# Optimization experiments

Hardware: AMD Instinct MI355X
Metric: run time of the kernel (lower is better)

## Reference

```python
import jax, jax.numpy as jnp
import numpy as np


def setup_inputs() -> dict:
    key = jax.random.key(0)
    N, L, S, H, E = 2, 2048, 2048, 8, 64
    k0, k1, k2, k3 = jax.random.split(key, 4)
    queries = jax.random.normal(k0, (N, L, H, E), dtype=jnp.float32)
    keys = jax.random.normal(k1, (N, S, H, E), dtype=jnp.float32)
    values = jax.random.normal(k2, (N, S, H, E), dtype=jnp.float32)
    Erel = jax.random.normal(k3, (L, E), dtype=jnp.float32)  # self.E relative embedding table
    # causal additive mask: 0 where key <= query, -1e9 elsewhere
    attn_mask_add = jnp.where(jnp.arange(S)[None, :] <= jnp.arange(L)[:, None], 0.0, -1e9).astype(jnp.float32)
    key_len_add = jnp.zeros((N, S), dtype=jnp.float32)  # full-length sequences
    return {"queries": queries, "keys": keys, "values": values, "Erel": Erel,
            "attn_mask_add": attn_mask_add, "key_len_add": key_len_add}


def reference(queries, keys, values, Erel, attn_mask_add, key_len_add):
    N, L, H, E = queries.shape
    S = keys.shape[1]
    temp = 1.0 / np.sqrt(E)
    q = (queries * temp).transpose(0, 2, 1, 3)   # [N,H,L,E]
    k = keys.transpose(0, 2, 1, 3)               # [N,H,S,E]
    # relative logits: QE [N,H,L,M], M = L (E table has L rows)
    QE = jnp.einsum('nhle,me->nhlm', q, Erel)
    M = QE.shape[-1]
    # _qe_masking: keep qe[i, j] where j >= M - 1 - i
    i = jnp.arange(L)[:, None]
    j = jnp.arange(M)[None, :]
    QE = QE * (j >= (M - 1 - i)).astype(QE.dtype)
    # _skewing: pad one zero column on the left, reshape swapping last two dims, drop first row
    padded = jnp.pad(QE, ((0, 0), (0, 0), (0, 0), (1, 0)))          # [N,H,L,M+1]
    Srel = padded.reshape(N, H, M + 1, L)[:, :, 1:, :]               # [N,H,M,L] == [N,H,L,S] since M==L==S
    QK = (jnp.einsum('nhle,nhse->nhls', q, k)
          + Srel
          + attn_mask_add[None, None, :, :]
          + key_len_add[:, None, None, :])
    A = jax.nn.softmax(QK, axis=-1)  # dropout disabled (eval-mode reference)
    V = jnp.einsum('nhls,nshd->nlhd', A, values)
    return V
```

## Files before the change

kernel.cpp:

```cpp
#include <hip/hip_runtime.h>
#include <hip/hip_bf16.h>


typedef __attribute__((ext_vector_type(8))) short bf16x8;
typedef __attribute__((ext_vector_type(4))) float f32x4;
typedef unsigned short u16;

#define L_Q 2048
#define S_K 2048
#define N_H 8
#define E_D 64
#define RSTRIDE 512
#define LOG2E 1.44269504088896f

#define QW_OFF 0u
#define KW_OFF (4u << 20)
#define VT_OFF (8u << 20)
#define EW_OFF (12u << 20)
#define ML_OFF (13u << 20)
#define OW_OFF ((13u << 20) + (512u << 10))
#define WS_PACK ((size_t)(13u << 20))
#define WS_FULL ((size_t)OW_OFF + (size_t)1024 * 4096 * 4)

static __device__ __forceinline__ short f2bf(float f) {
  unsigned u = __builtin_bit_cast(unsigned, f);
  u += 0x7fffu + ((u >> 16) & 1u);
  return (short)(u >> 16);
}

static __device__ __forceinline__ unsigned pk2(float a, float b) {
  return (unsigned)(u16)f2bf(a) | ((unsigned)(u16)f2bf(b) << 16);
}

static __device__ __forceinline__ bf16x8 loadpack8(const float* __restrict__ p, float scale) {
  float4 a = *reinterpret_cast<const float4*>(p);
  float4 b = *reinterpret_cast<const float4*>(p + 4);
  bf16x8 r;
  r[0] = f2bf(a.x * scale); r[1] = f2bf(a.y * scale);
  r[2] = f2bf(a.z * scale); r[3] = f2bf(a.w * scale);
  r[4] = f2bf(b.x * scale); r[5] = f2bf(b.y * scale);
  r[6] = f2bf(b.z * scale); r[7] = f2bf(b.w * scale);
  return r;
}

__global__ __launch_bounds__(256)
void pack_qke(const float* __restrict__ Qf, const float* __restrict__ Kf,
              const float* __restrict__ Ef, u16* __restrict__ Qw,
              u16* __restrict__ Kw, u16* __restrict__ Ew) {
  const unsigned u = blockIdx.x * 256 + threadIdx.x;
  if (u < 1048576u) {
    const unsigned v  = u & 524287u;
    const int e  = (v & 15) * 4;
    const int i  = (v >> 4) & 2047;
    const int nh = v >> 15;
    const int n = nh >> 3, h = nh & 7;
    const size_t src = ((size_t)(n * L_Q + i) * N_H + h) * E_D + e;
    const size_t dst = ((size_t)nh * L_Q + i) * E_D + e;
    const bool isQ = u < 524288u;
    float4 x = *reinterpret_cast<const float4*>((isQ ? Qf : Kf) + src);
    const float s = isQ ? 0.125f * LOG2E : 1.0f;
    ushort4 o;
    o.x = (u16)f2bf(x.x * s); o.y = (u16)f2bf(x.y * s);
    o.z = (u16)f2bf(x.z * s); o.w = (u16)f2bf(x.w * s);
    *reinterpret_cast<ushort4*>((isQ ? Qw : Kw) + dst) = o;
  } else {
    const unsigned v = u - 1048576u;
    if (v < 32768u) {
      const size_t idx = (size_t)v * 4;
      float4 x = *reinterpret_cast<const float4*>(Ef + idx);
      ushort4 o;
      o.x = (u16)f2bf(x.x); o.y = (u16)f2bf(x.y);
      o.z = (u16)f2bf(x.z); o.w = (u16)f2bf(x.w);
      *reinterpret_cast<ushort4*>(Ew + idx) = o;
    }
  }
}

__global__ __launch_bounds__(256)
void pack_vt(const float* __restrict__ Vf, u16* __restrict__ Vtw) {
  __shared__ u16 t[64][72];
  const int j0 = blockIdx.x * 64;
  const int nh = blockIdx.y;
  const int n = nh >> 3, h = nh & 7;
  const int tid = threadIdx.x;
  {
    const int jr = tid >> 2, dg = (tid & 3) * 16;
    const float* src = Vf + ((size_t)(n * L_Q + j0 + jr) * N_H + h) * E_D + dg;
#pragma unroll
    for (int q = 0; q < 4; ++q) {
      float4 x = *reinterpret_cast<const float4*>(src + q * 4);
      t[jr][dg + q * 4 + 0] = (u16)f2bf(x.x);
      t[jr][dg + q * 4 + 1] = (u16)f2bf(x.y);
      t[jr][dg + q * 4 + 2] = (u16)f2bf(x.z);
      t[jr][dg + q * 4 + 3] = (u16)f2bf(x.w);
    }
  }
  __syncthreads();
  {
    const int dr = tid >> 2, jg = (tid & 3) * 16;
    u16 tmp[16];
#pragma unroll
    for (int jj = 0; jj < 16; ++jj) tmp[jj] = t[jg + jj][dr];
    u16* dst = Vtw + ((size_t)nh * E_D + dr) * S_K + j0 + jg;
    *reinterpret_cast<uint4*>(dst)     = *reinterpret_cast<uint4*>(&tmp[0]);
    *reinterpret_cast<uint4*>(dst + 8) = *reinterpret_cast<uint4*>(&tmp[8]);
  }
}

template <bool SPLIT>
__global__ __launch_bounds__(256, 3)
void relattn_r11(const u16* __restrict__ Qw, const u16* __restrict__ Kw,
                 const u16* __restrict__ Vtw, const u16* __restrict__ Ew,
                 const float* __restrict__ KLp, float* __restrict__ Op,
                 float* __restrict__ OwP, float* __restrict__ MLp) {
  const int bid = blockIdx.x;
  const int nh = bid & 15;
  const int n = nh >> 3, h = nh & 7;
  const int rest = bid >> 4;
  const int wq64 = SPLIT ? (31 - (rest >> 1))
                         : ((rest < 16) ? (31 - rest) : (rest - 16));
  const int sp = SPLIT ? (rest & 1) : 0;
  const int iw64 = wq64 * 64;
  const int tid = threadIdx.x;
  const int wid = tid >> 6;
  const int lane = tid & 63;
  const int lo = lane & 15, hi = lane >> 4;
  const int iw = iw64 + wid * 16;
  const int nt = wq64 + 1;
  const int t0 = (SPLIT && sp) ? (nt >> 1) : 0;
  const int t1 = (SPLIT && !sp) ? (nt >> 1) : nt;
  const int s = (wq64 * 16 + nh) * 2 + sp;

  __shared__ u16 Kls[2][64 * 64];
  __shared__ u16 Vls[2][64 * 64];
  __shared__ float qe_lds[4][16 * 80];

  if (SPLIT && t0 >= t1) {
    f32x4 z = {};
    f32x4* OwF = reinterpret_cast<f32x4*>(OwP) + (size_t)s * 1024 + wid * 256 + lane;
#pragma unroll
    for (int dt = 0; dt < 4; ++dt) OwF[dt * 64] = z;
    if (lane < 16) {
      MLp[s * 128 + wid * 32 + lane] = -1e30f;
      MLp[s * 128 + wid * 32 + 16 + lane] = 0.f;
    }
    return;
  }

  const u16* Kg = Kw + (size_t)nh * S_K * E_D;
  const u16* Vg = Vtw + (size_t)nh * E_D * S_K;
  const float* klq = KLp + (size_t)n * S_K + 4 * hi;
  const u16* epl = Ew + (size_t)(2032 - iw) * E_D + lo * E_D + hi * 8;

  const int srow = lane >> 3;
  const int scc  = lane & 7;
  const int r0 = wid * 8 + srow;
  const int r1 = r0 + 32;
  const int swc = (scc ^ srow) * 8;
  uint4 stK[2], stV[2];

  auto LOAD_KV = [&](int jj0) {
    stK[0] = *reinterpret_cast<const uint4*>(Kg + (size_t)(jj0 + r0) * E_D + scc * 8);
    stK[1] = *reinterpret_cast<const uint4*>(Kg + (size_t)(jj0 + r1) * E_D + scc * 8);
    stV[0] = *reinterpret_cast<const uint4*>(Vg + (size_t)r0 * S_K + jj0 + scc * 8);
    stV[1] = *reinterpret_cast<const uint4*>(Vg + (size_t)r1 * S_K + jj0 + scc * 8);
  };
  auto WRITE_KV = [&](int bb) {
    *reinterpret_cast<uint4*>(&Kls[bb][r0 * 64 + swc]) = stK[0];
    *reinterpret_cast<uint4*>(&Kls[bb][r1 * 64 + swc]) = stK[1];
    *reinterpret_cast<uint4*>(&Vls[bb][r0 * 64 + swc]) = stV[0];
    *reinterpret_cast<uint4*>(&Vls[bb][r1 * 64 + swc]) = stV[1];
  };

  bf16x8 efc[8];
  auto LOAD_EFC = [&](int tt64) {
#pragma unroll
    for (int kt = 0; kt < 2; ++kt)
#pragma unroll
      for (int tt = 1; tt < 5; ++tt)
        efc[kt * 4 + tt - 1] = *reinterpret_cast<const bf16x8*>(
            epl + (size_t)(tt64 * 64 + tt * 16) * E_D + kt * 32);
  };

  bf16x8 qa[2];
  {
    const u16* qrow = Qw + ((size_t)nh * L_Q + iw + lo) * E_D + hi * 8;
    qa[0] = *reinterpret_cast<const bf16x8*>(qrow);
    qa[1] = *reinterpret_cast<const bf16x8*>(qrow + 32);
  }

  LOAD_KV(t0 * 64);
  WRITE_KV(0);
  if (t0 + 1 < t1) LOAD_KV((t0 + 1) * 64);
  LOAD_EFC(t0);
  __syncthreads();

  f32x4 o_acc[4] = {};
  float m_run = -1e30f, l_run = 0.f;
  const float* rb = &qe_lds[wid][lo * 80 + (15 - lo) + 4 * hi];
  const int lsw = lo & 7;
  int b = 0;
  f32x4 qe_carry = {};

  for (int t = t0; t < t1; ++t) {
    const int j0 = t * 64;
    if (t + 1 < t1) WRITE_KV(b ^ 1);
    if (t + 2 < t1) LOAD_KV(j0 + 128);

    __builtin_amdgcn_s_setprio(1);
    f32x4 s_acc[4] = {};
#pragma unroll
    for (int kt = 0; kt < 2; ++kt)
#pragma unroll
      for (int ct = 0; ct < 4; ++ct) {
        const bf16x8 kf = *reinterpret_cast<const bf16x8*>(
            &Kls[b][(ct * 16 + lo) * 64 + (((kt * 4 + hi) ^ lsw) * 8)]);
        s_acc[ct] = __builtin_amdgcn_mfma_f32_16x16x32_bf16(kf, qa[kt], s_acc[ct], 0, 0, 0);
      }

    f32x4 qe_acc[5];
    if (t == t0) {
      f32x4 z = {};
      qe_acc[0] = z;
#pragma unroll
      for (int kt = 0; kt < 2; ++kt) {
        const bf16x8 e0 = *reinterpret_cast<const bf16x8*>(
            epl + (size_t)(t0 * 64) * E_D + kt * 32);
        qe_acc[0] = __builtin_amdgcn_mfma_f32_16x16x32_bf16(e0, qa[kt], qe_acc[0], 0, 0, 0);
      }
    } else {
      qe_acc[0] = qe_carry;
    }
#pragma unroll
    for (int tt = 1; tt < 5; ++tt) { f32x4 z = {}; qe_acc[tt] = z; }
#pragma unroll
    for (int kt = 0; kt < 2; ++kt)
#pragma unroll
      for (int tt = 1; tt < 5; ++tt)
        qe_acc[tt] = __builtin_amdgcn_mfma_f32_16x16x32_bf16(efc[kt * 4 + tt - 1], qa[kt],
                                                             qe_acc[tt], 0, 0, 0);
    qe_carry = qe_acc[4];
    __builtin_amdgcn_s_setprio(0);

    if (t + 1 < t1) LOAD_EFC(t + 1);

#pragma unroll
    for (int tt = 0; tt < 5; ++tt)
      *reinterpret_cast<f32x4*>(&qe_lds[wid][lo * 80 + tt * 16 + 4 * hi]) = qe_acc[tt];

    float4 klv[4];
#pragma unroll
    for (int ct = 0; ct < 4; ++ct)
      klv[ct] = *reinterpret_cast<const float4*>(klq + j0 + ct * 16);

    const bool maskt = (t == nt - 1);
    const int thr = iw + lo - j0 - 4 * hi;
    float p[4][4];
#pragma unroll
    for (int ct = 0; ct < 4; ++ct) {
      const float k0 = klv[ct].x * LOG2E, k1 = klv[ct].y * LOG2E;
      const float k2 = klv[ct].z * LOG2E, k3 = klv[ct].w * LOG2E;
      p[ct][0] = s_acc[ct][0] + rb[ct * 16 + 0] + k0;
      p[ct][1] = s_acc[ct][1] + rb[ct * 16 + 1] + k1;
      p[ct][2] = s_acc[ct][2] + rb[ct * 16 + 2] + k2;
      p[ct][3] = s_acc[ct][3] + rb[ct * 16 + 3] + k3;
      if (maskt) {
#pragma unroll
        for (int g = 0; g < 4; ++g)
          if (ct * 16 + g > thr) p[ct][g] = -1e30f;
      }
    }

    float a0 = fmaxf(fmaxf(p[0][0], p[0][1]), fmaxf(p[0][2], p[0][3]));
    float a1 = fmaxf(fmaxf(p[1][0], p[1][1]), fmaxf(p[1][2], p[1][3]));
    float a2 = fmaxf(fmaxf(p[2][0], p[2][1]), fmaxf(p[2][2], p[2][3]));
    float a3 = fmaxf(fmaxf(p[3][0], p[3][1]), fmaxf(p[3][2], p[3][3]));
    float tmax = fmaxf(fmaxf(a0, a1), fmaxf(a2, a3));
    tmax = fmaxf(tmax, __shfl_xor(tmax, 16));
    tmax = fmaxf(tmax, __shfl_xor(tmax, 32));
    const float mnew = fmaxf(m_run, tmax);
    const float alpha = exp2f(m_run - mnew);
#pragma unroll
    for (int ct = 0; ct < 4; ++ct)
#pragma unroll
      for (int g = 0; g < 4; ++g)
        p[ct][g] = exp2f(p[ct][g] - mnew);
    float s0 = (p[0][0] + p[0][1]) + (p[0][2] + p[0][3]);
    float s1 = (p[1][0] + p[1][1]) + (p[1][2] + p[1][3]);
    float s2 = (p[2][0] + p[2][1]) + (p[2][2] + p[2][3]);
    float s3 = (p[3][0] + p[3][1]) + (p[3][2] + p[3][3]);
    float rs = (s0 + s1) + (s2 + s3);
    rs += __shfl_xor(rs, 16);
    rs += __shfl_xor(rs, 32);
    l_run = l_run * alpha + rs;
    m_run = mnew;

#pragma unroll
    for (int dt = 0; dt < 4; ++dt) o_acc[dt] = o_acc[dt] * alpha;

    uint4 w0, w1;
    w0.x = pk2(p[0][0], p[0][1]); w0.y = pk2(p[0][2], p[0][3]);
    w0.z = pk2(p[1][0], p[1][1]); w0.w = pk2(p[1][2], p[1][3]);
    w1.x = pk2(p[2][0], p[2][1]); w1.y = pk2(p[2][2], p[2][3]);
    w1.z = pk2(p[3][0], p[3][1]); w1.w = pk2(p[3][2], p[3][3]);
    const bf16x8 pb0 = __builtin_bit_cast(bf16x8, w0);
    const bf16x8 pb1 = __builtin_bit_cast(bf16x8, w1);

    __builtin_amdgcn_s_setprio(1);
#pragma unroll
    for (int kt = 0; kt < 2; ++kt)
#pragma unroll
      for (int dt = 0; dt < 4; ++dt) {
        const int vrow = dt * 16 + lo;
        const int ch = kt * 4 + (hi >> 1);
        const uint2 va2 = *reinterpret_cast<const uint2*>(
            &Vls[b][vrow * 64 + ((ch ^ lsw) * 8) + (hi & 1) * 4]);
        const uint2 vb2 = *reinterpret_cast<const uint2*>(
            &Vls[b][vrow * 64 + (((ch + 2) ^ lsw) * 8) + (hi & 1) * 4]);
        uint4 uw; uw.x = va2.x; uw.y = va2.y; uw.z = vb2.x; uw.w = vb2.y;
        const bf16x8 vf = __builtin_bit_cast(bf16x8, uw);
        o_acc[dt] = __builtin_amdgcn_mfma_f32_16x16x32_bf16(vf, kt ? pb1 : pb0, o_acc[dt], 0, 0, 0);
      }
    __builtin_amdgcn_s_setprio(0);

    __syncthreads();
    b ^= 1;
  }

  if (SPLIT) {
    f32x4* OwF = reinterpret_cast<f32x4*>(OwP) + (size_t)s * 1024 + wid * 256 + lane;
#pragma unroll
    for (int dt = 0; dt < 4; ++dt) OwF[dt * 64] = o_acc[dt];
    if (lane < 16) {
      MLp[s * 128 + wid * 32 + lane] = m_run;
      MLp[s * 128 + wid * 32 + 16 + lane] = l_run;
    }
  } else {
    const float inv = 1.f / l_run;
    float* ob = Op + (size_t)n * L_Q * RSTRIDE + h * E_D + (size_t)(iw + lo) * RSTRIDE;
#pragma unroll
    for (int dt = 0; dt < 4; ++dt) {
      f32x4 o = o_acc[dt] * inv;
      *reinterpret_cast<f32x4*>(ob + dt * 16 + 4 * hi) = o;
    }
  }
}

__global__ __launch_bounds__(256)
void combine64(const float* __restrict__ OwP, const float* __restrict__ MLp,
               float* __restrict__ Op) {
  const int pair = blockIdx.x;
  const int nh = pair & 15;
  const int wq64 = pair >> 4;
  const int n = nh >> 3, h = nh & 7;
  const int tid = threadIdx.x;
  const int wid = tid >> 6;
  const int lane = tid & 63;
  const int lo = lane & 15, hi = lane >> 4;
  const int s0 = pair * 2, s1 = s0 + 1;
  const float m0 = MLp[s0 * 128 + wid * 32 + lo], l0 = MLp[s0 * 128 + wid * 32 + 16 + lo];
  const float m1 = MLp[s1 * 128 + wid * 32 + lo], l1 = MLp[s1 * 128 + wid * 32 + 16 + lo];
  const float M  = fmaxf(m0, m1);
  const float w0 = exp2f(m0 - M), w1 = exp2f(m1 - M);
  const float inv = 1.f / (l0 * w0 + l1 * w1);
  const f32x4* A = reinterpret_cast<const f32x4*>(OwP) + (size_t)s0 * 1024 + wid * 256 + lane;
  const f32x4* B = reinterpret_cast<const f32x4*>(OwP) + (size_t)s1 * 1024 + wid * 256 + lane;
  float* ob = Op + (size_t)n * L_Q * RSTRIDE + h * E_D
            + (size_t)(wq64 * 64 + wid * 16 + lo) * RSTRIDE;
#pragma unroll
  for (int dt = 0; dt < 4; ++dt) {
    f32x4 o = (A[dt * 64] * w0 + B[dt * 64] * w1) * inv;
    *reinterpret_cast<f32x4*>(ob + dt * 16 + 4 * hi) = o;
  }
}

__global__ __launch_bounds__(64, 2)
void relattn_fb(const float* __restrict__ Qf, const float* __restrict__ Kf,
                const float* __restrict__ Vf, const float* __restrict__ Ef,
                const float* __restrict__ KLp, float* __restrict__ Op) {
  const int bid = blockIdx.x;
  const int nh = bid & 15;
  const int n = nh >> 3, h = nh & 7;
  const int wq = 127 - (bid >> 4);
  const int iw = wq * 16;
  const int lane = threadIdx.x & 63;
  const int lo = lane & 15, hi = lane >> 4;

  __shared__ u16 p_lds[16 * 72];

  const float* klp = KLp + (size_t)n * S_K;
  float* ob = Op + (size_t)n * L_Q * RSTRIDE + h * E_D;

  bf16x8 qa[2];
  const float* qb = Qf + ((size_t)(n * L_Q + iw + lo) * N_H + h) * E_D + hi * 8;
  qa[0] = loadpack8(qb, 0.125f);
  qa[1] = loadpack8(qb + 32, 0.125f);

  f32x4 o_acc[4] = {};
  float m_run[4], l_run[4];
#pragma unroll
  for (int g = 0; g < 4; ++g) { m_run[g] = -1e30f; l_run[g] = 0.f; }

  const int ntiles = (wq >> 2) + 1;
  for (int t = 0; t < ntiles; ++t) {
    const int j0 = t * 64;
    f32x4 s_acc[4] = {};
#pragma unroll
    for (int kt = 0; kt < 2; ++kt)
#pragma unroll
      for (int ct = 0; ct < 4; ++ct) {
        bf16x8 kf = loadpack8(Kf + ((size_t)(n * S_K + j0 + ct * 16 + lo) * N_H + h) * E_D
                                  + kt * 32 + hi * 8, 1.f);
        s_acc[ct] = __builtin_amdgcn_mfma_f32_16x16x32_bf16(qa[kt], kf, s_acc[ct], 0, 0, 0);
      }
    const int mbase = (L_Q - 1) - (iw + 15) + j0;
    f32x4 qe_acc[5] = {};
#pragma unroll
    for (int kt = 0; kt < 2; ++kt)
#pragma unroll
      for (int tt = 0; tt < 5; ++tt) {
        int mr = mbase + tt * 16 + lo;
        mr = mr > (L_Q - 1) ? (L_Q - 1) : mr;
        bf16x8 ef = loadpack8(Ef + (size_t)mr * E_D + kt * 32 + hi * 8, 1.f);
        qe_acc[tt] = __builtin_amdgcn_mfma_f32_16x16x32_bf16(qa[kt], ef, qe_acc[tt], 0, 0, 0);
      }
    float kladd[4];
#pragma unroll
    for (int ct = 0; ct < 4; ++ct) kladd[ct] = klp[j0 + ct * 16 + lo];
    float sv[4][4];
#pragma unroll
    for (int ct = 0; ct < 4; ++ct) {
      const int jj = ct * 16 + lo;
#pragma unroll
      for (int g = 0; g < 4; ++g) {
        const int r = 4 * hi + g;
        const int u = jj - r + 15;
        const int srcl = (u & 15) | (hi << 4);
        const float a = __shfl(qe_acc[ct][g], srcl);
        const float bq = __shfl(qe_acc[ct + 1][g], srcl);
        const float rel = (lo <= r) ? a : bq;
        float sv2 = s_acc[ct][g] + rel + kladd[ct];
        if (j0 + jj > iw + r) sv2 = -1e9f;
        sv[ct][g] = sv2;
      }
    }
    float alpha[4];
#pragma unroll
    for (int g = 0; g < 4; ++g) {
      float mx = fmaxf(fmaxf(sv[0][g], sv[1][g]), fmaxf(sv[2][g], sv[3][g]));
      mx = fmaxf(mx, __shfl_xor(mx, 1));
      mx = fmaxf(mx, __shfl_xor(mx, 2));
      mx = fmaxf(mx, __shfl_xor(mx, 4));
      mx = fmaxf(mx, __shfl_xor(mx, 8));
      const float mnew = fmaxf(m_run[g], mx);
      const float al = __expf(m_run[g] - mnew);
      float rsv = 0.f;
#pragma unroll
      for (int ct = 0; ct < 4; ++ct) {
        const float pv = __expf(sv[ct][g] - mnew);
        sv[ct][g] = pv;
        rsv += pv;
      }
      rsv += __shfl_xor(rsv, 1);
      rsv += __shfl_xor(rsv, 2);
      rsv += __shfl_xor(rsv, 4);
      rsv += __shfl_xor(rsv, 8);
      l_run[g] = l_run[g] * al + rsv;
      m_run[g] = mnew;
      alpha[g] = al;
    }
#pragma unroll
    for (int dt = 0; dt < 4; ++dt)
#pragma unroll
      for (int g = 0; g < 4; ++g)
        o_acc[dt][g] *= alpha[g];
#pragma unroll
    for (int ct = 0; ct < 4; ++ct)
#pragma unroll
      for (int g = 0; g < 4; ++g)
        p_lds[(4 * hi + g) * 72 + ct * 16 + lo] = (u16)f2bf(sv[ct][g]);
#pragma unroll
    for (int jt = 0; jt < 2; ++jt) {
      const bf16x8 pav = *reinterpret_cast<const bf16x8*>(&p_lds[lo * 72 + jt * 32 + hi * 8]);
#pragma unroll
      for (int dt = 0; dt < 4; ++dt) {
        bf16x8 vf;
        const float* vp = Vf + ((size_t)(n * S_K + j0 + jt * 32 + hi * 8) * N_H + h) * E_D
                            + dt * 16 + lo;
#pragma unroll
        for (int e = 0; e < 8; ++e) vf[e] = f2bf(vp[(size_t)e * RSTRIDE]);
        o_acc[dt] = __builtin_amdgcn_mfma_f32_16x16x32_bf16(pav, vf, o_acc[dt], 0, 0, 0);
      }
    }
  }
  float inv[4];
#pragma unroll
  for (int g = 0; g < 4; ++g) inv[g] = 1.f / l_run[g];
#pragma unroll
  for (int dt = 0; dt < 4; ++dt)
#pragma unroll
    for (int g = 0; g < 4; ++g)
      ob[(size_t)(iw + 4 * hi + g) * RSTRIDE + dt * 16 + lo] = o_acc[dt][g] * inv[g];
}

extern "C" void kernel_launch(void* const* d_in, const int* in_sizes, int n_in,
                              void* d_out, int out_size, void* d_ws, size_t ws_size,
                              hipStream_t stream) {
  const float* Q  = (const float*)d_in[0];
  const float* K  = (const float*)d_in[1];
  const float* V  = (const float*)d_in[2];
  const float* E  = (const float*)d_in[3];
  const float* KL = (const float*)d_in[5];
  float* O = (float*)d_out;

  char* ws = (char*)d_ws;
  u16* Qw   = (u16*)(ws + QW_OFF);
  u16* Kw   = (u16*)(ws + KW_OFF);
  u16* Vtw  = (u16*)(ws + VT_OFF);
  u16* Ew   = (u16*)(ws + EW_OFF);
  float* ML = (float*)(ws + ML_OFF);
  float* Ow = (float*)(ws + OW_OFF);

  const bool ws_pack = ws_size >= WS_PACK;
  const bool ws_full = ws_size >= WS_FULL;

  if (ws_pack) {
    hipLaunchKernelGGL(pack_qke, dim3((1048576 + 32768 + 255) / 256), dim3(256), 0, stream,
                       Q, K, E, Qw, Kw, Ew);
    hipLaunchKernelGGL(pack_vt, dim3(32, 16), dim3(256), 0, stream, V, Vtw);
  }
  if (ws_full) {
    hipLaunchKernelGGL((relattn_r11<true>), dim3(1024), dim3(256), 0, stream,
                       Qw, Kw, Vtw, Ew, KL, O, Ow, ML);
    hipLaunchKernelGGL(combine64, dim3(512), dim3(256), 0, stream, Ow, ML, O);
  } else if (ws_pack) {
    hipLaunchKernelGGL((relattn_r11<false>), dim3(512), dim3(256), 0, stream,
                       Qw, Kw, Vtw, Ew, KL, O, Ow, ML);
  } else {
    hipLaunchKernelGGL(relattn_fb, dim3(2048), dim3(64), 0, stream, Q, K, V, E, KL, O);
  }
}
```

Baseline: 93.57 us.

## Move the loop barrier mid-iteration and prefetch key-length bias one tile ahead

All V fragment reads from LDS now happen before a new mid-iteration barrier. That barrier waits on lgkmcnt and replaces the trailing __syncthreads, so each loop iteration has one barrier placed where its wait can overlap softmax work. The key-length bias for the next tile is also loaded one iteration early into registers. The cost is 16 extra uint2 registers holding V fragments plus the prefetched bias, which could push register pressure past the 3-blocks-per-CU launch bound.

New measurement: 104.9 us. 1.12x slower.

```diff
diff --git a/kernel.cpp b/kernel.cpp
--- a/kernel.cpp
+++ b/kernel.cpp
@@ -21,6 +21,13 @@
 #define OW_OFF ((13u << 20) + (512u << 10))
 #define WS_PACK ((size_t)(13u << 20))
 #define WS_FULL ((size_t)OW_OFF + (size_t)1024 * 4096 * 4)
+
+static __device__ __forceinline__ void barrier_lgkm() {
+  asm volatile("s_waitcnt lgkmcnt(0)" ::: "memory");
+  __builtin_amdgcn_sched_barrier(0);
+  __builtin_amdgcn_s_barrier();
+  __builtin_amdgcn_sched_barrier(0);
+}
 
 static __device__ __forceinline__ short f2bf(float f) {
   unsigned u = __builtin_bit_cast(unsigned, f);
@@ -109,7 +116,7 @@
 
 template <bool SPLIT>
 __global__ __launch_bounds__(256, 3)
-void relattn_r11(const u16* __restrict__ Qw, const u16* __restrict__ Kw,
+void relattn_r12(const u16* __restrict__ Qw, const u16* __restrict__ Kw,
                  const u16* __restrict__ Vtw, const u16* __restrict__ Ew,
                  const float* __restrict__ KLp, float* __restrict__ Op,
                  float* __restrict__ OwP, float* __restrict__ MLp) {
@@ -182,6 +189,13 @@
             epl + (size_t)(tt64 * 64 + tt * 16) * E_D + kt * 32);
   };
 
+  float4 klvn[4];
+  auto LOAD_KLV = [&](int jj0) {
+#pragma unroll
+    for (int ct = 0; ct < 4; ++ct)
+      klvn[ct] = *reinterpret_cast<const float4*>(klq + jj0 + ct * 16);
+  };
+
   bf16x8 qa[2];
   {
     const u16* qrow = Qw + ((size_t)nh * L_Q + iw + lo) * E_D + hi * 8;
@@ -193,7 +207,8 @@
   WRITE_KV(0);
   if (t0 + 1 < t1) LOAD_KV((t0 + 1) * 64);
   LOAD_EFC(t0);
-  __syncthreads();
+  LOAD_KLV(t0 * 64);
+  barrier_lgkm();
 
   f32x4 o_acc[4] = {};
   float m_run = -1e30f, l_run = 0.f;
@@ -248,10 +263,25 @@
     for (int tt = 0; tt < 5; ++tt)
       *reinterpret_cast<f32x4*>(&qe_lds[wid][lo * 80 + tt * 16 + 4 * hi]) = qe_acc[tt];
 
+    uint2 vva[8], vvb[8];
+#pragma unroll
+    for (int kt = 0; kt < 2; ++kt)
+#pragma unroll
+      for (int dt = 0; dt < 4; ++dt) {
+        const int vrow = dt * 16 + lo;
+        const int ch = kt * 4 + (hi >> 1);
+        vva[kt * 4 + dt] = *reinterpret_cast<const uint2*>(
+            &Vls[b][vrow * 64 + ((ch ^ lsw) * 8) + (hi & 1) * 4]);
+        vvb[kt * 4 + dt] = *reinterpret_cast<const uint2*>(
+            &Vls[b][vrow * 64 + (((ch + 2) ^ lsw) * 8) + (hi & 1) * 4]);
+      }
+
     float4 klv[4];
 #pragma unroll
-    for (int ct = 0; ct < 4; ++ct)
-      klv[ct] = *reinterpret_cast<const float4*>(klq + j0 + ct * 16);
+    for (int ct = 0; ct < 4; ++ct) klv[ct] = klvn[ct];
+    if (t + 1 < t1) LOAD_KLV(j0 + 64);
+
+    barrier_lgkm();
 
     const bool maskt = (t == nt - 1);
     const int thr = iw + lo - j0 - 4 * hi;
@@ -311,19 +341,14 @@
     for (int kt = 0; kt < 2; ++kt)
 #pragma unroll
       for (int dt = 0; dt < 4; ++dt) {
-        const int vrow = dt * 16 + lo;
-        const int ch = kt * 4 + (hi >> 1);
-        const uint2 va2 = *reinterpret_cast<const uint2*>(
-            &Vls[b][vrow * 64 + ((ch ^ lsw) * 8) + (hi & 1) * 4]);
-        const uint2 vb2 = *reinterpret_cast<const uint2*>(
-            &Vls[b][vrow * 64 + (((ch + 2) ^ lsw) * 8) + (hi & 1) * 4]);
-        uint4 uw; uw.x = va2.x; uw.y = va2.y; uw.z = vb2.x; uw.w = vb2.y;
+        uint4 uw;
+        uw.x = vva[kt * 4 + dt].x; uw.y = vva[kt * 4 + dt].y;
+        uw.z = vvb[kt * 4 + dt].x; uw.w = vvb[kt * 4 + dt].y;
         const bf16x8 vf = __builtin_bit_cast(bf16x8, uw);
         o_acc[dt] = __builtin_amdgcn_mfma_f32_16x16x32_bf16(vf, kt ? pb1 : pb0, o_acc[dt], 0, 0, 0);
       }
     __builtin_amdgcn_s_setprio(0);
 
-    __syncthreads();
     b ^= 1;
   }
 
@@ -530,11 +555,11 @@
     hipLaunchKernelGGL(pack_vt, dim3(32, 16), dim3(256), 0, stream, V, Vtw);
   }
   if (ws_full) {
-    hipLaunchKernelGGL((relattn_r11<true>), dim3(1024), dim3(256), 0, stream,
+    hipLaunchKernelGGL((relattn_r12<true>), dim3(1024), dim3(256), 0, stream,
                        Qw, Kw, Vtw, Ew, KL, O, Ow, ML);
     hipLaunchKernelGGL(combine64, dim3(512), dim3(256), 0, stream, Ow, ML, O);
   } else if (ws_pack) {
-    hipLaunchKernelGGL((relattn_r11<false>), dim3(512), dim3(256), 0, stream,
+    hipLaunchKernelGGL((relattn_r12<false>), dim3(512), dim3(256), 0, stream,
                        Qw, Kw, Vtw, Ew, KL, O, Ow, ML);
   } else {
     hipLaunchKernelGGL(relattn_fb, dim3(2048), dim3(64), 0, stream, Q, K, V, E, KL, O);
```

## Load V fragments directly from global into registers, drop V LDS staging

Applied to the files above, without the earlier changes.

V tiles are no longer staged through double-buffered shared memory. Each lane now reads its V MFMA fragments straight from global memory (8-byte loads) into registers early in each iteration, so the latency hides behind the QK and QE work. This removes the V LDS buffer, and with it LDS footprint and write/read traffic, which allows raising launch bounds to 4 blocks per CU. The risks are many narrow, uncoalesced global loads per iteration, more register pressure under the tighter occupancy bound, and heavier reliance on the cache.

Result: slower. 195.6 us (+109.0%).

```diff
diff --git a/kernel.cpp b/kernel.cpp
--- a/kernel.cpp
+++ b/kernel.cpp
@@ -108,8 +108,8 @@
 }
 
 template <bool SPLIT>
-__global__ __launch_bounds__(256, 3)
-void relattn_r11(const u16* __restrict__ Qw, const u16* __restrict__ Kw,
+__global__ __launch_bounds__(256, 4)
+void relattn_r13(const u16* __restrict__ Qw, const u16* __restrict__ Kw,
                  const u16* __restrict__ Vtw, const u16* __restrict__ Ew,
                  const float* __restrict__ KLp, float* __restrict__ Op,
                  float* __restrict__ OwP, float* __restrict__ MLp) {
@@ -132,7 +132,6 @@
   const int s = (wq64 * 16 + nh) * 2 + sp;
 
   __shared__ u16 Kls[2][64 * 64];
-  __shared__ u16 Vls[2][64 * 64];
   __shared__ float qe_lds[4][16 * 80];
 
   if (SPLIT && t0 >= t1) {
@@ -151,25 +150,22 @@
   const u16* Vg = Vtw + (size_t)nh * E_D * S_K;
   const float* klq = KLp + (size_t)n * S_K + 4 * hi;
   const u16* epl = Ew + (size_t)(2032 - iw) * E_D + lo * E_D + hi * 8;
+  const u16* vpl = Vg + (size_t)lo * S_K + 4 * hi;
 
   const int srow = lane >> 3;
   const int scc  = lane & 7;
   const int r0 = wid * 8 + srow;
   const int r1 = r0 + 32;
   const int swc = (scc ^ srow) * 8;
-  uint4 stK[2], stV[2];
-
-  auto LOAD_KV = [&](int jj0) {
+  uint4 stK[2];
+
+  auto LOAD_K = [&](int jj0) {
     stK[0] = *reinterpret_cast<const uint4*>(Kg + (size_t)(jj0 + r0) * E_D + scc * 8);
     stK[1] = *reinterpret_cast<const uint4*>(Kg + (size_t)(jj0 + r1) * E_D + scc * 8);
-    stV[0] = *reinterpret_cast<const uint4*>(Vg + (size_t)r0 * S_K + jj0 + scc * 8);
-    stV[1] = *reinterpret_cast<const uint4*>(Vg + (size_t)r1 * S_K + jj0 + scc * 8);
   };
-  auto WRITE_KV = [&](int bb) {
+  auto WRITE_K = [&](int bb) {
     *reinterpret_cast<uint4*>(&Kls[bb][r0 * 64 + swc]) = stK[0];
     *reinterpret_cast<uint4*>(&Kls[bb][r1 * 64 + swc]) = stK[1];
-    *reinterpret_cast<uint4*>(&Vls[bb][r0 * 64 + swc]) = stV[0];
-    *reinterpret_cast<uint4*>(&Vls[bb][r1 * 64 + swc]) = stV[1];
   };
 
   bf16x8 efc[8];
@@ -189,9 +185,9 @@
     qa[1] = *reinterpret_cast<const bf16x8*>(qrow + 32);
   }
 
-  LOAD_KV(t0 * 64);
-  WRITE_KV(0);
-  if (t0 + 1 < t1) LOAD_KV((t0 + 1) * 64);
+  LOAD_K(t0 * 64);
+  WRITE_K(0);
+  if (t0 + 1 < t1) LOAD_K((t0 + 1) * 64);
   LOAD_EFC(t0);
   __syncthreads();
 
@@ -204,8 +200,8 @@
 
   for (int t = t0; t < t1; ++t) {
     const int j0 = t * 64;
-    if (t + 1 < t1) WRITE_KV(b ^ 1);
-    if (t + 2 < t1) LOAD_KV(j0 + 128);
+    if (t + 1 < t1) WRITE_K(b ^ 1);
+    if (t + 2 < t1) LOAD_K(j0 + 128);
 
     __builtin_amdgcn_s_setprio(1);
     f32x4 s_acc[4] = {};
@@ -217,7 +213,19 @@
             &Kls[b][(ct * 16 + lo) * 64 + (((kt * 4 + hi) ^ lsw) * 8)]);
         s_acc[ct] = __builtin_amdgcn_mfma_f32_16x16x32_bf16(kf, qa[kt], s_acc[ct], 0, 0, 0);
       }
-
+    __builtin_amdgcn_s_setprio(0);
+
+    ushort4 va4[8], vb4[8];
+#pragma unroll
+    for (int kt = 0; kt < 2; ++kt)
+#pragma unroll
+      for (int dt = 0; dt < 4; ++dt) {
+        const u16* vp = vpl + (size_t)(dt * 16) * S_K + j0 + kt * 32;
+        va4[kt * 4 + dt] = *reinterpret_cast<const ushort4*>(vp);
+        vb4[kt * 4 + dt] = *reinterpret_cast<const ushort4*>(vp + 16);
+      }
+
+    __builtin_amdgcn_s_setprio(1);
     f32x4 qe_acc[5];
     if (t == t0) {
       f32x4 z = {};
@@ -311,14 +319,11 @@
     for (int kt = 0; kt < 2; ++kt)
 #pragma unroll
       for (int dt = 0; dt < 4; ++dt) {
-        const int vrow = dt * 16 + lo;
-        const int ch = kt * 4 + (hi >> 1);
-        const uint2 va2 = *reinterpret_cast<const uint2*>(
-            &Vls[b][vrow * 64 + ((ch ^ lsw) * 8) + (hi & 1) * 4]);
-        const uint2 vb2 = *reinterpret_cast<const uint2*>(
-            &Vls[b][vrow * 64 + (((ch + 2) ^ lsw) * 8) + (hi & 1) * 4]);
-        uint4 uw; uw.x = va2.x; uw.y = va2.y; uw.z = vb2.x; uw.w = vb2.y;
-        const bf16x8 vf = __builtin_bit_cast(bf16x8, uw);
+        const ushort4 a = va4[kt * 4 + dt];
+        const ushort4 bb = vb4[kt * 4 + dt];
+        bf16x8 vf;
+        vf[0] = (short)a.x;  vf[1] = (short)a.y;  vf[2] = (short)a.z;  vf[3] = (short)a.w;
+        vf[4] = (short)bb.x; vf[5] = (short)bb.y; vf[6] = (short)bb.z; vf[7] = (short)bb.w;
         o_acc[dt] = __builtin_amdgcn_mfma_f32_16x16x32_bf16(vf, kt ? pb1 : pb0, o_acc[dt], 0, 0, 0);
       }
     __builtin_amdgcn_s_setprio(0);
@@ -530,11 +535,11 @@
     hipLaunchKernelGGL(pack_vt, dim3(32, 16), dim3(256), 0, stream, V, Vtw);
   }
   if (ws_full) {
-    hipLaunchKernelGGL((relattn_r11<true>), dim3(1024), dim3(256), 0, stream,
+    hipLaunchKernelGGL((relattn_r13<true>), dim3(1024), dim3(256), 0, stream,
                        Qw, Kw, Vtw, Ew, KL, O, Ow, ML);
     hipLaunchKernelGGL(combine64, dim3(512), dim3(256), 0, stream, Ow, ML, O);
   } else if (ws_pack) {
-    hipLaunchKernelGGL((relattn_r11<false>), dim3(512), dim3(256), 0, stream,
+    hipLaunchKernelGGL((relattn_r13<false>), dim3(512), dim3(256), 0, stream,
                        Qw, Kw, Vtw, Ew, KL, O, Ow, ML);
   } else {
     hipLaunchKernelGGL(relattn_fb, dim3(2048), dim3(64), 0, stream, Q, K, V, E, KL, O);
```

## Split causal attention KV range four ways and store partials as bf16

Applied to the files above, without the earlier changes.

The split-KV attention kernel now divides each 64-row query tile's key range into four chunks instead of two, launching 2048 blocks, and a combine kernel merges the four partials with log-sum-exp weights. Partial outputs are stored as bf16 instead of fp32 to keep the larger partial buffer within workspace and cut write and read traffic. This aims at better load balance and occupancy for the triangular causal workload. It adds more partial traffic and combine work, and rounding partial outputs to bf16 reduces accuracy.

Result: no change. 94.20 us (+0.7%).

```diff
diff --git a/kernel.cpp b/kernel.cpp
--- a/kernel.cpp
+++ b/kernel.cpp
@@ -17,15 +17,19 @@
 #define KW_OFF (4u << 20)
 #define VT_OFF (8u << 20)
 #define EW_OFF (12u << 20)
-#define ML_OFF (13u << 20)
+#define ML_OFF ((12u << 20) + (512u << 10))
 #define OW_OFF ((13u << 20) + (512u << 10))
-#define WS_PACK ((size_t)(13u << 20))
-#define WS_FULL ((size_t)OW_OFF + (size_t)1024 * 4096 * 4)
+#define WS_PACK ((size_t)ML_OFF)
+#define WS_FULL ((size_t)OW_OFF + (size_t)2048 * 4096 * 2)
 
 static __device__ __forceinline__ short f2bf(float f) {
   unsigned u = __builtin_bit_cast(unsigned, f);
   u += 0x7fffu + ((u >> 16) & 1u);
   return (short)(u >> 16);
+}
+
+static __device__ __forceinline__ float bf2f(u16 u) {
+  return __builtin_bit_cast(float, ((unsigned)u) << 16);
 }
 
 static __device__ __forceinline__ unsigned pk2(float a, float b) {
@@ -109,17 +113,17 @@
 
 template <bool SPLIT>
 __global__ __launch_bounds__(256, 3)
-void relattn_r11(const u16* __restrict__ Qw, const u16* __restrict__ Kw,
+void relattn_r14(const u16* __restrict__ Qw, const u16* __restrict__ Kw,
                  const u16* __restrict__ Vtw, const u16* __restrict__ Ew,
                  const float* __restrict__ KLp, float* __restrict__ Op,
-                 float* __restrict__ OwP, float* __restrict__ MLp) {
+                 u16* __restrict__ OwP, float* __restrict__ MLp) {
   const int bid = blockIdx.x;
   const int nh = bid & 15;
   const int n = nh >> 3, h = nh & 7;
   const int rest = bid >> 4;
-  const int wq64 = SPLIT ? (31 - (rest >> 1))
+  const int wq64 = SPLIT ? (31 - (rest >> 2))
                          : ((rest < 16) ? (31 - rest) : (rest - 16));
-  const int sp = SPLIT ? (rest & 1) : 0;
+  const int sp = SPLIT ? (rest & 3) : 0;
   const int iw64 = wq64 * 64;
   const int tid = threadIdx.x;
   const int wid = tid >> 6;
@@ -127,19 +131,20 @@
   const int lo = lane & 15, hi = lane >> 4;
   const int iw = iw64 + wid * 16;
   const int nt = wq64 + 1;
-  const int t0 = (SPLIT && sp) ? (nt >> 1) : 0;
-  const int t1 = (SPLIT && !sp) ? (nt >> 1) : nt;
-  const int s = (wq64 * 16 + nh) * 2 + sp;
+  const int t0 = SPLIT ? ((sp * nt) >> 2) : 0;
+  const int t1 = SPLIT ? (((sp + 1) * nt) >> 2) : nt;
+  const int s = (wq64 * 16 + nh) * 4 + sp;
 
   __shared__ u16 Kls[2][64 * 64];
   __shared__ u16 Vls[2][64 * 64];
   __shared__ float qe_lds[4][16 * 80];
 
   if (SPLIT && t0 >= t1) {
-    f32x4 z = {};
-    f32x4* OwF = reinterpret_cast<f32x4*>(OwP) + (size_t)s * 1024 + wid * 256 + lane;
-#pragma unroll
-    for (int dt = 0; dt < 4; ++dt) OwF[dt * 64] = z;
+    u16* OwH = OwP + (size_t)s * 4096 + wid * 1024 + lane * 4;
+    ushort4 z4 = {0, 0, 0, 0};
+#pragma unroll
+    for (int dt = 0; dt < 4; ++dt)
+      *reinterpret_cast<ushort4*>(OwH + dt * 256) = z4;
     if (lane < 16) {
       MLp[s * 128 + wid * 32 + lane] = -1e30f;
       MLp[s * 128 + wid * 32 + 16 + lane] = 0.f;
@@ -328,9 +333,14 @@
   }
 
   if (SPLIT) {
-    f32x4* OwF = reinterpret_cast<f32x4*>(OwP) + (size_t)s * 1024 + wid * 256 + lane;
-#pragma unroll
-    for (int dt = 0; dt < 4; ++dt) OwF[dt * 64] = o_acc[dt];
+    u16* OwH = OwP + (size_t)s * 4096 + wid * 1024 + lane * 4;
+#pragma unroll
+    for (int dt = 0; dt < 4; ++dt) {
+      ushort4 o4;
+      o4.x = (u16)f2bf(o_acc[dt][0]); o4.y = (u16)f2bf(o_acc[dt][1]);
+      o4.z = (u16)f2bf(o_acc[dt][2]); o4.w = (u16)f2bf(o_acc[dt][3]);
+      *reinterpret_cast<ushort4*>(OwH + dt * 256) = o4;
+    }
     if (lane < 16) {
       MLp[s * 128 + wid * 32 + lane] = m_run;
       MLp[s * 128 + wid * 32 + 16 + lane] = l_run;
@@ -347,8 +357,8 @@
 }
 
 __global__ __launch_bounds__(256)
-void combine64(const float* __restrict__ OwP, const float* __restrict__ MLp,
-               float* __restrict__ Op) {
+void combine4(const u16* __restrict__ Owh, const float* __restrict__ MLp,
+              float* __restrict__ Op) {
   const int pair = blockIdx.x;
   const int nh = pair & 15;
   const int wq64 = pair >> 4;
@@ -357,19 +367,35 @@
   const int wid = tid >> 6;
   const int lane = tid & 63;
   const int lo = lane & 15, hi = lane >> 4;
-  const int s0 = pair * 2, s1 = s0 + 1;
-  const float m0 = MLp[s0 * 128 + wid * 32 + lo], l0 = MLp[s0 * 128 + wid * 32 + 16 + lo];
-  const float m1 = MLp[s1 * 128 + wid * 32 + lo], l1 = MLp[s1 * 128 + wid * 32 + 16 + lo];
-  const float M  = fmaxf(m0, m1);
-  const float w0 = exp2f(m0 - M), w1 = exp2f(m1 - M);
-  const float inv = 1.f / (l0 * w0 + l1 * w1);
-  const f32x4* A = reinterpret_cast<const f32x4*>(OwP) + (size_t)s0 * 1024 + wid * 256 + lane;
-  const f32x4* B = reinterpret_cast<const f32x4*>(OwP) + (size_t)s1 * 1024 + wid * 256 + lane;
+  const int sb = pair * 4;
+
+  float m[4], l[4];
+#pragma unroll
+  for (int i = 0; i < 4; ++i) {
+    m[i] = MLp[(sb + i) * 128 + wid * 32 + lo];
+    l[i] = MLp[(sb + i) * 128 + wid * 32 + 16 + lo];
+  }
+  float M = fmaxf(fmaxf(m[0], m[1]), fmaxf(m[2], m[3]));
+  float w[4]; float den = 0.f;
+#pragma unroll
+  for (int i = 0; i < 4; ++i) { w[i] = exp2f(m[i] - M); den += l[i] * w[i]; }
+  const float inv = 1.f / den;
+
   float* ob = Op + (size_t)n * L_Q * RSTRIDE + h * E_D
             + (size_t)(wq64 * 64 + wid * 16 + lo) * RSTRIDE;
 #pragma unroll
   for (int dt = 0; dt < 4; ++dt) {
-    f32x4 o = (A[dt * 64] * w0 + B[dt * 64] * w1) * inv;
+    f32x4 acc = {};
+#pragma unroll
+    for (int i = 0; i < 4; ++i) {
+      const ushort4 v = *reinterpret_cast<const ushort4*>(
+          Owh + (size_t)(sb + i) * 4096 + wid * 1024 + dt * 256 + lane * 4);
+      acc[0] += w[i] * bf2f(v.x);
+      acc[1] += w[i] * bf2f(v.y);
+      acc[2] += w[i] * bf2f(v.z);
+      acc[3] += w[i] * bf2f(v.w);
+    }
+    f32x4 o = acc * inv;
     *reinterpret_cast<f32x4*>(ob + dt * 16 + 4 * hi) = o;
   }
 }
@@ -519,7 +545,7 @@
   u16* Vtw  = (u16*)(ws + VT_OFF);
   u16* Ew   = (u16*)(ws + EW_OFF);
   float* ML = (float*)(ws + ML_OFF);
-  float* Ow = (float*)(ws + OW_OFF);
+  u16* Ow   = (u16*)(ws + OW_OFF);
 
   const bool ws_pack = ws_size >= WS_PACK;
   const bool ws_full = ws_size >= WS_FULL;
@@ -530,11 +556,11 @@
     hipLaunchKernelGGL(pack_vt, dim3(32, 16), dim3(256), 0, stream, V, Vtw);
   }
   if (ws_full) {
-    hipLaunchKernelGGL((relattn_r11<true>), dim3(1024), dim3(256), 0, stream,
+    hipLaunchKernelGGL((relattn_r14<true>), dim3(2048), dim3(256), 0, stream,
                        Qw, Kw, Vtw, Ew, KL, O, Ow, ML);
-    hipLaunchKernelGGL(combine64, dim3(512), dim3(256), 0, stream, Ow, ML, O);
+    hipLaunchKernelGGL(combine4, dim3(512), dim3(256), 0, stream, Ow, ML, O);
   } else if (ws_pack) {
-    hipLaunchKernelGGL((relattn_r11<false>), dim3(512), dim3(256), 0, stream,
+    hipLaunchKernelGGL((relattn_r14<false>), dim3(512), dim3(256), 0, stream,
                        Qw, Kw, Vtw, Ew, KL, O, Ow, ML);
   } else {
     hipLaunchKernelGGL(relattn_fb, dim3(2048), dim3(64), 0, stream, Q, K, V, E, KL, O);
```
